# Optimization experiments

Hardware: AMD Instinct MI355X
Metric: run time of the kernel (lower is better)

Reference implementation:

```python
import jax, jax.numpy as jnp
import numpy as np

H_DIM = 64; GRID = 8; G = GRID * GRID; NEIGH = 2.0
ATT = 1024; EMB = 4
S = 32; P = 64; B = S * P


def setup_inputs() -> dict:
    key = jax.random.key(0)
    ks = jax.random.split(key, 20)
    bounds = jnp.arange(0, B + 1, P, dtype=jnp.int32)
    seq_start_end = jnp.stack([bounds[:-1], bounds[1:]], axis=1)  # (S,2) uniform scenes
    def lin(k, fan_in, shape):
        return jax.random.normal(k, shape, jnp.float32) / np.sqrt(fan_in)
    return {
        "h_states": jax.random.normal(ks[0], (1, B, H_DIM), jnp.float32),
        "seq_start_end": seq_start_end,
        "end_pos": jax.random.uniform(ks[1], (B, 2), jnp.float32) * 4.0,
        "rel_pos": jax.random.normal(ks[2], (B, 2), jnp.float32),
        # Attention_Decoder params
        "W_enc": lin(ks[3], H_DIM, (H_DIM, ATT)), "b_enc": jnp.zeros((ATT,), jnp.float32),
        "W_dec": lin(ks[4], H_DIM, (H_DIM, ATT)), "b_dec": jnp.zeros((ATT,), jnp.float32),
        "w_full": lin(ks[5], ATT, (ATT,)), "b_full": jnp.zeros((), jnp.float32),
        "W_embed": lin(ks[6], 4, (4, EMB)), "b_embed": jnp.zeros((EMB,), jnp.float32),
        "W_out": lin(ks[7], H_DIM + EMB, (H_DIM + EMB, ATT)), "b_out": jnp.zeros((ATT,), jnp.float32),
        # mlp_pool params (Linear -> BatchNorm -> ReLU)
        "W_mlp": lin(ks[8], ATT, (ATT, ATT)), "b_mlp": jnp.zeros((ATT,), jnp.float32),
        "bn_gamma": jnp.ones((ATT,), jnp.float32), "bn_beta": jnp.zeros((ATT,), jnp.float32),
    }


def social_pool(h, end_pos):
    # h: (B, H), end_pos: (B, 2); uniform scenes S x P
    pos = end_pos.reshape(S, P, 2)
    hid = h.reshape(S, P, H_DIM)
    ax = pos[:, :, None, 0]; ay = pos[:, :, None, 1]  # anchor (S,P,1)
    ox = pos[:, None, :, 0]; oy = pos[:, None, :, 1]  # other  (S,1,P)
    half = NEIGH / 2
    tl_x = ax - half; tl_y = ay + half
    br_x = ax + half; br_y = ay - half
    cell_x = jnp.floor((ox - tl_x) / NEIGH * GRID)
    cell_y = jnp.floor((tl_y - oy) / NEIGH * GRID)
    grid = (cell_x + cell_y * GRID).astype(jnp.int32)  # (S,P,P)
    oob = (ox >= br_x) | (ox <= tl_x) | (oy >= tl_y) | (oy <= br_y)
    oob = oob | jnp.eye(P, dtype=bool)[None]  # self-pairs excluded (within_bound[0::P+1]=1)
    anchor_off = (jnp.arange(P, dtype=jnp.int32) * G)[None, :, None]
    idx = jnp.where(oob, 0, grid + 1 + anchor_off)  # slot 0 = dump slot
    seq_off = (jnp.arange(S, dtype=jnp.int32) * (P * G + 1))[:, None, None]
    flat_idx = (idx + seq_off).reshape(-1)
    vals = jnp.broadcast_to(hid[:, None, :, :], (S, P, P, H_DIM)).reshape(-1, H_DIM)
    buf = jnp.zeros((S * (P * G + 1), H_DIM), h.dtype).at[flat_idx].add(vals)
    buf = buf.reshape(S, P * G + 1, H_DIM)[:, 1:, :]  # drop dump slot per scene
    return buf.reshape(B, G, H_DIM)


def reference(h_states, seq_start_end, end_pos, rel_pos,
              W_enc, b_enc, W_dec, b_dec, w_full, b_full,
              W_embed, b_embed, W_out, b_out, W_mlp, b_mlp, bn_gamma, bn_beta):
    del seq_start_end  # uniform scene layout baked into S, P
    h = h_states.reshape(-1, H_DIM)                      # (B, H)
    enc = social_pool(h, end_pos)                        # (B, G, H)
    dec_a = h @ W_dec + b_dec                            # (B, ATT)
    enc_a = jnp.einsum('bgh,ha->bga', enc, W_enc) + b_enc
    scores = jax.nn.relu(enc_a + dec_a[:, None, :]) @ w_full + b_full  # (B, G)
    alpha = jax.nn.softmax(scores, axis=-1)
    ctx = jnp.einsum('bg,bgh->bh', alpha, enc)           # (B, H)
    embed_info = jnp.concatenate([end_pos, rel_pos], axis=1)  # (B, 4)
    emb = jax.nn.relu(embed_info @ W_embed + b_embed)
    out = jax.nn.relu(jnp.concatenate([ctx, emb], axis=1) @ W_out + b_out)  # (B, ATT)
    # mlp_pool: Linear -> BatchNorm1d (training-mode batch stats) -> ReLU
    x = out @ W_mlp + b_mlp
    mu = jnp.mean(x, axis=0)
    var = jnp.var(x, axis=0)
    x = (x - mu) * jax.lax.rsqrt(var + 1e-5) * bn_gamma + bn_beta
    return jax.nn.relu(x)
```

## Files before the change

kernel.cpp:

```cpp
#include <hip/hip_runtime.h>
#include <hip/hip_bf16.h>
#include <math.h>

#define H_DIM 64
#define G 64
#define ATT 1024
#define EMB 4
#define P 64
#define BB 2048
#define MAXROWS 129088
#define PREP_BLOCKS (2048 + 16 + 16 + 16 + 256)

typedef __attribute__((ext_vector_type(8))) short short8;
typedef __attribute__((ext_vector_type(4))) float floatx4;

__device__ inline ushort f2bf(float v) {
    __hip_bfloat16 b = __float2bfloat16(v);
    return *(ushort*)&b;
}
__device__ inline float bf2f(ushort u) {
    union { float f; unsigned u32; } x;
    x.u32 = ((unsigned)u) << 16;
    return x.f;
}

__global__ __launch_bounds__(256) void prep_kernel(const float* __restrict__ h,
                                                   const float* __restrict__ end_pos,
                                                   const float* __restrict__ W_enc,
                                                   const float* __restrict__ W_dec,
                                                   const float* __restrict__ W_out,
                                                   const float* __restrict__ W_mlp,
                                                   ushort* __restrict__ enc,
                                                   ushort* __restrict__ h_bf,
                                                   ushort* __restrict__ Wte,
                                                   ushort* __restrict__ Wdt,
                                                   ushort* __restrict__ Wot,
                                                   ushort* __restrict__ Wt,
                                                   int* __restrict__ rowidx,
                                                   int* __restrict__ cntA,
                                                   int* __restrict__ baseA,
                                                   int* __restrict__ counter) {
    __shared__ float cellp[2][G][H_DIM];
    __shared__ float tileT[64][65];
    __shared__ unsigned long long hitsS[2];
    __shared__ int baseS;

    int blk = blockIdx.x;
    int t = threadIdx.x;

    if (blk < 2048) {
        int b = blk, s = b >> 6, i = b & 63;
        int w = t >> 6, lane = t & 63;
        float* cp = &cellp[0][0][0];
        #pragma unroll
        for (int idx = 0; idx < 8; ++idx)
            *(float4*)&cp[(t + 256 * idx) * 4] = (float4){0.f, 0.f, 0.f, 0.f};
        if (w == 3) h_bf[(size_t)b * 64 + lane] = f2bf(h[(size_t)b * 64 + lane]);
        __syncthreads();

        float ax = end_pos[2 * b], ay = end_pos[2 * b + 1];
        float tlx = ax - 1.f, tly = ay + 1.f, brx = ax + 1.f, bry = ay - 1.f;
        const float* hseq = h + (size_t)s * P * H_DIM;
        const float* pseq = end_pos + (size_t)s * P * 2;

        if (w < 2) {
            unsigned long long hits = 0ull;
            for (int jj = 0; jj < 32; ++jj) {
                int j = w * 32 + jj;
                float ox = pseq[2 * j], oy = pseq[2 * j + 1];
                bool oob = (ox >= brx) || (ox <= tlx) || (oy >= tly) || (oy <= bry) || (j == i);
                if (!oob) {
                    int cx = (int)floorf((ox - tlx) / 2.0f * 8.0f);
                    int cy = (int)floorf((tly - oy) / 2.0f * 8.0f);
                    int g = cx + cy * 8;
                    hits |= (1ull << g);
                    cellp[w][g][lane] += hseq[j * H_DIM + lane];
                }
            }
            if (lane == 0) hitsS[w] = hits;
        }
        __syncthreads();
        unsigned long long uh = hitsS[0] | hitsS[1];
        int n_nz = __popcll(uh);
        if (t == 0) {
            int bs = atomicAdd(counter, n_nz);
            baseS = bs; cntA[b] = n_nz; baseA[b] = bs;
        }
        __syncthreads();
        int base = baseS;
        for (int g = w; g < 64; g += 4) {
            if ((uh >> g) & 1ull) {
                int slot = __popcll(uh & ((1ull << g) - 1ull));
                enc[((size_t)(b * G + g)) * H_DIM + lane] =
                    f2bf(cellp[0][g][lane] + cellp[1][g][lane]);
                if (lane == 0) rowidx[base + slot] = b * G + g;
            }
        }
    } else if (blk < 2064) {
        int n0 = (blk - 2048) * 64;
        #pragma unroll
        for (int idx = 0; idx < 16; ++idx) {
            int flat = t + 256 * idx;
            int k = flat >> 6, c = flat & 63;
            tileT[k][c] = W_enc[(size_t)k * ATT + n0 + c];
        }
        __syncthreads();
        #pragma unroll
        for (int idx = 0; idx < 16; ++idx) {
            int flat = t + 256 * idx;
            int n = flat >> 6, k = flat & 63;
            Wte[(size_t)(n0 + n) * 64 + k] = f2bf(tileT[k][n]);
        }
    } else if (blk < 2080) {
        int n0 = (blk - 2064) * 64;
        #pragma unroll
        for (int idx = 0; idx < 16; ++idx) {
            int flat = t + 256 * idx;
            int k = flat >> 6, c = flat & 63;
            tileT[k][c] = W_dec[(size_t)k * ATT + n0 + c];
        }
        __syncthreads();
        #pragma unroll
        for (int idx = 0; idx < 16; ++idx) {
            int flat = t + 256 * idx;
            int n = flat >> 6, k = flat & 63;
            Wdt[(size_t)(n0 + n) * 64 + k] = f2bf(tileT[k][n]);
        }
    } else if (blk < 2096) {
        int n0 = (blk - 2080) * 64;
        int n = t & 63, kg = t >> 6;
        #pragma unroll
        for (int kk = 0; kk < 24; ++kk) {
            int k = kg * 24 + kk;
            float v = (k < 68) ? W_out[(size_t)k * ATT + n0 + n] : 0.f;
            Wot[(size_t)(n0 + n) * 96 + k] = f2bf(v);
        }
    } else {
        int idx2 = blk - 2096;
        int k0 = (idx2 & 15) * 64, n0 = (idx2 >> 4) * 64;
        #pragma unroll
        for (int idx = 0; idx < 16; ++idx) {
            int flat = t + 256 * idx;
            int r = flat >> 6, c = flat & 63;
            tileT[r][c] = W_mlp[(size_t)(k0 + r) * ATT + n0 + c];
        }
        __syncthreads();
        #pragma unroll
        for (int idx = 0; idx < 16; ++idx) {
            int flat = t + 256 * idx;
            int r = flat >> 6, c = flat & 63;
            Wt[(size_t)(n0 + r) * ATT + k0 + c] = f2bf(tileT[c][r]);
        }
    }
}

__global__ __launch_bounds__(256) void dec_mfma_kernel(const ushort* __restrict__ A,
                                                       const ushort* __restrict__ Bt,
                                                       const float* __restrict__ b_dec,
                                                       const float* __restrict__ b_enc,
                                                       const float* __restrict__ w_full,
                                                       float* __restrict__ dec_r,
                                                       float* __restrict__ s_empty) {
    int t = threadIdx.x;
    int w = t >> 6, lane = t & 63;
    int lm = lane & 15, q = lane >> 4;
    int m0 = blockIdx.x * 64, n1 = blockIdx.y * 128;
    __shared__ __align__(16) ushort Asm[64][72];
    __shared__ __align__(16) ushort Bsm[128][72];

    #pragma unroll
    for (int i = 0; i < 4; ++i) {
        int flat = t + 256 * i;
        int r = flat >> 4, c4 = (flat & 15) * 4;
        *(uint2*)&Asm[r][c4] = *(const uint2*)&A[(size_t)(m0 + r) * 64 + c4];
    }
    #pragma unroll
    for (int i = 0; i < 8; ++i) {
        int flat = t + 256 * i;
        int r = flat >> 4, c4 = (flat & 15) * 4;
        *(uint2*)&Bsm[r][c4] = *(const uint2*)&Bt[(size_t)(n1 + r) * 64 + c4];
    }
    __syncthreads();

    floatx4 acc[4][2];
    #pragma unroll
    for (int mt = 0; mt < 4; ++mt)
        #pragma unroll
        for (int nt = 0; nt < 2; ++nt) acc[mt][nt] = (floatx4){0.f, 0.f, 0.f, 0.f};

    #pragma unroll
    for (int ks = 0; ks < 64; ks += 32) {
        short8 af[4], bfr[2];
        #pragma unroll
        for (int mt = 0; mt < 4; ++mt)
            af[mt] = *(const short8*)&Asm[mt * 16 + lm][ks + q * 8];
        #pragma unroll
        for (int nt = 0; nt < 2; ++nt)
            bfr[nt] = *(const short8*)&Bsm[w * 32 + nt * 16 + lm][ks + q * 8];
        #pragma unroll
        for (int mt = 0; mt < 4; ++mt)
            #pragma unroll
            for (int nt = 0; nt < 2; ++nt)
                acc[mt][nt] = __builtin_amdgcn_mfma_f32_16x16x32_bf16(af[mt], bfr[nt], acc[mt][nt], 0, 0, 0);
    }

    float part[4][4];
    #pragma unroll
    for (int mt = 0; mt < 4; ++mt)
        #pragma unroll
        for (int r = 0; r < 4; ++r) part[mt][r] = 0.f;

    #pragma unroll
    for (int nt = 0; nt < 2; ++nt) {
        int col = n1 + w * 32 + nt * 16 + lm;
        float bcol = b_dec[col] + b_enc[col];
        float wf = w_full[col];
        #pragma unroll
        for (int mt = 0; mt < 4; ++mt)
            #pragma unroll
            for (int r = 0; r < 4; ++r) {
                int row = m0 + mt * 16 + q * 4 + r;
                float v = acc[mt][nt][r] + bcol;
                dec_r[(size_t)row * ATT + col] = v;
                part[mt][r] += fmaxf(v, 0.f) * wf;
            }
    }
    #pragma unroll
    for (int mt = 0; mt < 4; ++mt)
        #pragma unroll
        for (int r = 0; r < 4; ++r) {
            float v = part[mt][r];
            v += __shfl_xor(v, 1); v += __shfl_xor(v, 2);
            v += __shfl_xor(v, 4); v += __shfl_xor(v, 8);
            part[mt][r] = v;
        }
    if (lm == 0) {
        #pragma unroll
        for (int mt = 0; mt < 4; ++mt)
            #pragma unroll
            for (int r = 0; r < 4; ++r)
                atomicAdd(&s_empty[m0 + mt * 16 + q * 4 + r], part[mt][r]);
    }
}

__global__ __launch_bounds__(256) void scoresC_mfma_kernel(const ushort* __restrict__ enc,
                                                           const int* __restrict__ rowidx,
                                                           const int* __restrict__ counter,
                                                           const float* __restrict__ dec_r,
                                                           const ushort* __restrict__ Wte,
                                                           const float* __restrict__ w_full,
                                                           const float* __restrict__ b_full,
                                                           float* __restrict__ score_c) {
    int M = counter[0];
    int row0 = blockIdx.x * 64;
    if (row0 >= M) return;
    int t = threadIdx.x;
    int w = t >> 6, lane = t & 63;
    int lm = lane & 15, q = lane >> 4;

    __shared__ __align__(16) ushort AS[64][72];
    __shared__ __align__(16) ushort BS[256][72];
    __shared__ int rowS[64];
    __shared__ float redS[4][64];

    if (t < 64) rowS[t] = (row0 + t < M) ? rowidx[row0 + t] : 0;
    __syncthreads();
    #pragma unroll
    for (int i = 0; i < 4; ++i) {
        int flat = t + 256 * i;
        int r = flat >> 4, c4 = (flat & 15) * 4;
        *(uint2*)&AS[r][c4] = *(const uint2*)&enc[(size_t)rowS[r] * 64 + c4];
    }
    int bbr[16];
    #pragma unroll
    for (int mt = 0; mt < 4; ++mt)
        #pragma unroll
        for (int r = 0; r < 4; ++r)
            bbr[mt * 4 + r] = rowS[mt * 16 + q * 4 + r] >> 6;

    float part[4][4];
    #pragma unroll
    for (int mt = 0; mt < 4; ++mt)
        #pragma unroll
        for (int r = 0; r < 4; ++r) part[mt][r] = 0.f;

    for (int c = 0; c < 4; ++c) {
        __syncthreads();
        #pragma unroll
        for (int i = 0; i < 16; ++i) {
            int flat = t + 256 * i;
            int r = flat >> 4, c4 = (flat & 15) * 4;
            *(uint2*)&BS[r][c4] = *(const uint2*)&Wte[(size_t)(c * 256 + r) * 64 + c4];
        }
        __syncthreads();

        floatx4 acc[4][4];
        #pragma unroll
        for (int mt = 0; mt < 4; ++mt)
            #pragma unroll
            for (int nt = 0; nt < 4; ++nt) acc[mt][nt] = (floatx4){0.f, 0.f, 0.f, 0.f};

        #pragma unroll
        for (int ks = 0; ks < 64; ks += 32) {
            short8 af[4], bfr[4];
            #pragma unroll
            for (int mt = 0; mt < 4; ++mt)
                af[mt] = *(const short8*)&AS[mt * 16 + lm][ks + q * 8];
            #pragma unroll
            for (int nt = 0; nt < 4; ++nt)
                bfr[nt] = *(const short8*)&BS[w * 64 + nt * 16 + lm][ks + q * 8];
            #pragma unroll
            for (int mt = 0; mt < 4; ++mt)
                #pragma unroll
                for (int nt = 0; nt < 4; ++nt)
                    acc[mt][nt] = __builtin_amdgcn_mfma_f32_16x16x32_bf16(af[mt], bfr[nt], acc[mt][nt], 0, 0, 0);
        }

        int colbase = c * 256 + w * 64;
        #pragma unroll
        for (int nt = 0; nt < 4; ++nt) {
            int col = colbase + nt * 16 + lm;
            float wf = w_full[col];
            #pragma unroll
            for (int mt = 0; mt < 4; ++mt)
                #pragma unroll
                for (int r = 0; r < 4; ++r) {
                    float v = acc[mt][nt][r] + dec_r[(size_t)bbr[mt * 4 + r] * ATT + col];
                    part[mt][r] += fmaxf(v, 0.f) * wf;
                }
        }
    }
    #pragma unroll
    for (int mt = 0; mt < 4; ++mt)
        #pragma unroll
        for (int r = 0; r < 4; ++r) {
            float v = part[mt][r];
            v += __shfl_xor(v, 1); v += __shfl_xor(v, 2);
            v += __shfl_xor(v, 4); v += __shfl_xor(v, 8);
            part[mt][r] = v;
        }
    if (lm == 0) {
        #pragma unroll
        for (int mt = 0; mt < 4; ++mt)
            #pragma unroll
            for (int r = 0; r < 4; ++r)
                redS[w][mt * 16 + q * 4 + r] = part[mt][r];
    }
    __syncthreads();
    if (t < 64) {
        int row = row0 + t;
        if (row < M)
            score_c[row] = redS[0][t] + redS[1][t] + redS[2][t] + redS[3][t] + b_full[0];
    }
}

__global__ __launch_bounds__(64) void softmax_ctx_kernel(const float* __restrict__ score_c,
                                                         const int* __restrict__ rowidx,
                                                         const int* __restrict__ cntA,
                                                         const int* __restrict__ baseA,
                                                         const float* __restrict__ s_empty,
                                                         const ushort* __restrict__ enc,
                                                         const float* __restrict__ end_pos,
                                                         const float* __restrict__ rel_pos,
                                                         const float* __restrict__ W_embed,
                                                         const float* __restrict__ b_embed,
                                                         const float* __restrict__ b_full,
                                                         ushort* __restrict__ ctx_bf) {
    int b = blockIdx.x, t = threadIdx.x;
    int cnt = cntA[b], base = baseA[b];
    float se = s_empty[b] + b_full[0];
    float sc = se;
    int ri = 0;
    if (t < cnt) { sc = score_c[base + t]; ri = rowidx[base + t]; }
    float mx = sc;
    #pragma unroll
    for (int o = 32; o > 0; o >>= 1) mx = fmaxf(mx, __shfl_xor(mx, o));
    float e = expf(sc - mx);
    float ssum = e;
    #pragma unroll
    for (int o = 32; o > 0; o >>= 1) ssum += __shfl_xor(ssum, o);
    __shared__ float aS[G];
    __shared__ int rS[G];
    aS[t] = e / ssum;
    rS[t] = ri;
    __syncthreads();
    float ctx = 0.f;
    for (int i = 0; i < cnt; ++i)
        ctx += aS[i] * bf2f(enc[(size_t)rS[i] * H_DIM + t]);
    ctx_bf[(size_t)b * 96 + t] = f2bf(ctx);
    if (t < EMB) {
        float e0 = end_pos[2*b], e1 = end_pos[2*b+1], e2 = rel_pos[2*b], e3 = rel_pos[2*b+1];
        float v = b_embed[t] + e0 * W_embed[0*EMB + t] + e1 * W_embed[1*EMB + t]
                             + e2 * W_embed[2*EMB + t] + e3 * W_embed[3*EMB + t];
        ctx_bf[(size_t)b * 96 + 64 + t] = f2bf(v > 0.f ? v : 0.f);
    }
    if (t < 28) ctx_bf[(size_t)b * 96 + 68 + t] = 0;
}

__global__ __launch_bounds__(256) void out_mfma_kernel(const ushort* __restrict__ A,
                                                       const ushort* __restrict__ Bt,
                                                       const float* __restrict__ bias,
                                                       ushort* __restrict__ out) {
    int t = threadIdx.x;
    int w = t >> 6, lane = t & 63;
    int lm = lane & 15, q = lane >> 4;
    int m0 = blockIdx.x * 64, n1 = blockIdx.y * 128;
    __shared__ __align__(16) ushort Asm[64][104];
    __shared__ __align__(16) ushort Bsm[128][104];

    {
        int r = t >> 2, pp = t & 3;
        #pragma unroll
        for (int ii = 0; ii < 3; ++ii) {
            int c8 = (pp * 3 + ii) * 8;
            *(uint4*)&Asm[r][c8] = *(const uint4*)&A[(size_t)(m0 + r) * 96 + c8];
        }
    }
    {
        int r = t >> 1, pp = t & 1;
        #pragma unroll
        for (int ii = 0; ii < 6; ++ii) {
            int c8 = (pp * 6 + ii) * 8;
            *(uint4*)&Bsm[r][c8] = *(const uint4*)&Bt[(size_t)(n1 + r) * 96 + c8];
        }
    }
    __syncthreads();

    floatx4 acc[4][2];
    #pragma unroll
    for (int mt = 0; mt < 4; ++mt)
        #pragma unroll
        for (int nt = 0; nt < 2; ++nt) acc[mt][nt] = (floatx4){0.f, 0.f, 0.f, 0.f};

    #pragma unroll
    for (int ks = 0; ks < 96; ks += 32) {
        short8 af[4], bfr[2];
        #pragma unroll
        for (int mt = 0; mt < 4; ++mt)
            af[mt] = *(const short8*)&Asm[mt * 16 + lm][ks + q * 8];
        #pragma unroll
        for (int nt = 0; nt < 2; ++nt)
            bfr[nt] = *(const short8*)&Bsm[w * 32 + nt * 16 + lm][ks + q * 8];
        #pragma unroll
        for (int mt = 0; mt < 4; ++mt)
            #pragma unroll
            for (int nt = 0; nt < 2; ++nt)
                acc[mt][nt] = __builtin_amdgcn_mfma_f32_16x16x32_bf16(af[mt], bfr[nt], acc[mt][nt], 0, 0, 0);
    }
    #pragma unroll
    for (int nt = 0; nt < 2; ++nt) {
        int col = n1 + w * 32 + nt * 16 + lm;
        float bv = bias[col];
        #pragma unroll
        for (int mt = 0; mt < 4; ++mt)
            #pragma unroll
            for (int r = 0; r < 4; ++r) {
                int row = m0 + mt * 16 + q * 4 + r;
                out[(size_t)row * ATT + col] = f2bf(fmaxf(acc[mt][nt][r] + bv, 0.f));
            }
    }
}

__global__ __launch_bounds__(256) void mlp_mfma_kernel(const ushort* __restrict__ A,
                                                       const ushort* __restrict__ Bt,
                                                       const float* __restrict__ bias,
                                                       float* __restrict__ X,
                                                       float* __restrict__ sums) {
    int t = threadIdx.x;
    int w = t >> 6, lane = t & 63;
    int lm = lane & 15, q = lane >> 4;
    int m0 = blockIdx.x * 64, n1 = blockIdx.y * 128;
    __shared__ __align__(16) ushort Asm[64][72];
    __shared__ __align__(16) ushort Bsm[128][72];

    floatx4 acc[4][2];
    #pragma unroll
    for (int mt = 0; mt < 4; ++mt)
        #pragma unroll
        for (int nt = 0; nt < 2; ++nt) acc[mt][nt] = (floatx4){0.f, 0.f, 0.f, 0.f};

    for (int k0 = 0; k0 < 1024; k0 += 64) {
        __syncthreads();
        #pragma unroll
        for (int i = 0; i < 4; ++i) {
            int flat = t + 256 * i;
            int r = flat >> 4, c4 = (flat & 15) * 4;
            *(uint2*)&Asm[r][c4] = *(const uint2*)&A[(size_t)(m0 + r) * 1024 + k0 + c4];
        }
        #pragma unroll
        for (int i = 0; i < 8; ++i) {
            int flat = t + 256 * i;
            int r = flat >> 4, c4 = (flat & 15) * 4;
            *(uint2*)&Bsm[r][c4] = *(const uint2*)&Bt[(size_t)(n1 + r) * 1024 + k0 + c4];
        }
        __syncthreads();
        #pragma unroll
        for (int ks = 0; ks < 64; ks += 32) {
            short8 af[4], bfr[2];
            #pragma unroll
            for (int mt = 0; mt < 4; ++mt)
                af[mt] = *(const short8*)&Asm[mt * 16 + lm][ks + q * 8];
            #pragma unroll
            for (int nt = 0; nt < 2; ++nt)
                bfr[nt] = *(const short8*)&Bsm[w * 32 + nt * 16 + lm][ks + q * 8];
            #pragma unroll
            for (int mt = 0; mt < 4; ++mt)
                #pragma unroll
                for (int nt = 0; nt < 2; ++nt)
                    acc[mt][nt] = __builtin_amdgcn_mfma_f32_16x16x32_bf16(af[mt], bfr[nt], acc[mt][nt], 0, 0, 0);
        }
    }
    #pragma unroll
    for (int nt = 0; nt < 2; ++nt) {
        int col = n1 + w * 32 + nt * 16 + lm;
        float bv = bias[col];
        float s1 = 0.f, s2 = 0.f;
        #pragma unroll
        for (int mt = 0; mt < 4; ++mt)
            #pragma unroll
            for (int r = 0; r < 4; ++r) {
                int row = m0 + mt * 16 + q * 4 + r;
                float v = acc[mt][nt][r] + bv;
                X[(size_t)row * 1024 + col] = v;
                s1 += v; s2 += v * v;
            }
        s1 += __shfl_xor(s1, 16); s1 += __shfl_xor(s1, 32);
        s2 += __shfl_xor(s2, 16); s2 += __shfl_xor(s2, 32);
        if (q == 0) {
            atomicAdd(&sums[col], s1);
            atomicAdd(&sums[ATT + col], s2);
        }
    }
}

__global__ __launch_bounds__(256) void bn_kernel(const float* __restrict__ X,
                                                 const float* __restrict__ sums,
                                                 const float* __restrict__ gamma,
                                                 const float* __restrict__ beta,
                                                 float* __restrict__ out) {
    size_t i = (size_t)blockIdx.x * 256 + threadIdx.x;
    int f = (int)(i & 1023);
    float mu = sums[f] * (1.f / BB);
    float var = sums[ATT + f] * (1.f / BB) - mu * mu;
    float v = (X[i] - mu) * rsqrtf(var + 1e-5f) * gamma[f] + beta[f];
    out[i] = v > 0.f ? v : 0.f;
}

extern "C" void kernel_launch(void* const* d_in, const int* in_sizes, int n_in,
                              void* d_out, int out_size, void* d_ws, size_t ws_size,
                              hipStream_t stream) {
    const float* h        = (const float*)d_in[0];
    const float* end_pos  = (const float*)d_in[2];
    const float* rel_pos  = (const float*)d_in[3];
    const float* W_enc    = (const float*)d_in[4];
    const float* b_enc    = (const float*)d_in[5];
    const float* W_dec    = (const float*)d_in[6];
    const float* b_dec    = (const float*)d_in[7];
    const float* w_full   = (const float*)d_in[8];
    const float* b_full   = (const float*)d_in[9];
    const float* W_embed  = (const float*)d_in[10];
    const float* b_embed  = (const float*)d_in[11];
    const float* W_out    = (const float*)d_in[12];
    const float* b_out    = (const float*)d_in[13];
    const float* W_mlp    = (const float*)d_in[14];
    const float* b_mlp    = (const float*)d_in[15];
    const float* bn_gamma = (const float*)d_in[16];
    const float* bn_beta  = (const float*)d_in[17];

    float* ws = (float*)d_ws;
    ushort* enc     = (ushort*)ws;
    ushort* h_bf    = (ushort*)(ws + 4194304);
    ushort* Wte     = (ushort*)(ws + 4259840);
    ushort* Wdt     = (ushort*)(ws + 4292608);
    ushort* Wot     = (ushort*)(ws + 4325376);
    ushort* Wt      = (ushort*)(ws + 4374528);
    ushort* ctx_bf  = (ushort*)(ws + 4898816);
    ushort* out_bf  = (ushort*)(ws + 4997120);
    float*  x       = ws + 6045696;
    float*  dec_r   = ws + 8388608;
    int*    rowidx  = (int*)(ws + 10485760);
    float*  score_c = ws + 10616832;
    int*    cntA    = (int*)(ws + 10747904);
    int*    baseA   = (int*)(ws + 10749952);
    int*    counter = (int*)(ws + 10752000);
    float*  s_empty = ws + 10752064;
    float*  sums    = ws + 10754112;

    hipMemsetAsync(counter, 0, (64 + 2048 + 2048) * sizeof(float), stream);

    prep_kernel<<<PREP_BLOCKS, 256, 0, stream>>>(h, end_pos, W_enc, W_dec, W_out, W_mlp,
                                                 enc, h_bf, Wte, Wdt, Wot, Wt,
                                                 rowidx, cntA, baseA, counter);
    dec_mfma_kernel<<<dim3(32, 8), 256, 0, stream>>>(h_bf, Wdt, b_dec, b_enc, w_full, dec_r, s_empty);
    scoresC_mfma_kernel<<<MAXROWS / 64, 256, 0, stream>>>(enc, rowidx, counter, dec_r, Wte,
                                                          w_full, b_full, score_c);
    softmax_ctx_kernel<<<BB, 64, 0, stream>>>(score_c, rowidx, cntA, baseA, s_empty, enc,
                                              end_pos, rel_pos, W_embed, b_embed, b_full, ctx_bf);
    out_mfma_kernel<<<dim3(32, 8), 256, 0, stream>>>(ctx_bf, Wot, b_out, out_bf);
    mlp_mfma_kernel<<<dim3(32, 8), 256, 0, stream>>>(out_bf, Wt, b_mlp, x, sums);
    bn_kernel<<<8192, 256, 0, stream>>>(x, sums, bn_gamma, bn_beta, (float*)d_out);
}
```

Baseline: 202.1 us.

## Compute social pooling per wavefront with ballot/shuffle instead of shared-memory cells

After: 195.7 us. 3.2% less time.

```diff
diff --git a/kernel.cpp b/kernel.cpp
--- a/kernel.cpp
+++ b/kernel.cpp
@@ -9,7 +9,7 @@
 #define P 64
 #define BB 2048
 #define MAXROWS 129088
-#define PREP_BLOCKS (2048 + 16 + 16 + 16 + 256)
+#define PREP_BLOCKS (512 + 16 + 16 + 16 + 256)
 
 typedef __attribute__((ext_vector_type(8))) short short8;
 typedef __attribute__((ext_vector_type(4))) float floatx4;
@@ -40,64 +40,57 @@
                                                    int* __restrict__ cntA,
                                                    int* __restrict__ baseA,
                                                    int* __restrict__ counter) {
-    __shared__ float cellp[2][G][H_DIM];
     __shared__ float tileT[64][65];
-    __shared__ unsigned long long hitsS[2];
-    __shared__ int baseS;
 
     int blk = blockIdx.x;
     int t = threadIdx.x;
 
-    if (blk < 2048) {
-        int b = blk, s = b >> 6, i = b & 63;
-        int w = t >> 6, lane = t & 63;
-        float* cp = &cellp[0][0][0];
-        #pragma unroll
-        for (int idx = 0; idx < 8; ++idx)
-            *(float4*)&cp[(t + 256 * idx) * 4] = (float4){0.f, 0.f, 0.f, 0.f};
-        if (w == 3) h_bf[(size_t)b * 64 + lane] = f2bf(h[(size_t)b * 64 + lane]);
-        __syncthreads();
-
-        float ax = end_pos[2 * b], ay = end_pos[2 * b + 1];
+    if (blk < 512) {
+        int wv = t >> 6, lane = t & 63;
+        int b = blk * 4 + wv;
+        int s = b >> 6, i = b & 63;
+        const float* pseq = end_pos + (size_t)s * P * 2;
+        const float* hrow = h + (size_t)s * P * H_DIM;
+
+        float2 pj = ((const float2*)pseq)[lane];
+        float ax = __shfl(pj.x, i), ay = __shfl(pj.y, i);
         float tlx = ax - 1.f, tly = ay + 1.f, brx = ax + 1.f, bry = ay - 1.f;
-        const float* hseq = h + (size_t)s * P * H_DIM;
-        const float* pseq = end_pos + (size_t)s * P * 2;
-
-        if (w < 2) {
-            unsigned long long hits = 0ull;
-            for (int jj = 0; jj < 32; ++jj) {
-                int j = w * 32 + jj;
-                float ox = pseq[2 * j], oy = pseq[2 * j + 1];
-                bool oob = (ox >= brx) || (ox <= tlx) || (oy >= tly) || (oy <= bry) || (j == i);
-                if (!oob) {
-                    int cx = (int)floorf((ox - tlx) / 2.0f * 8.0f);
-                    int cy = (int)floorf((tly - oy) / 2.0f * 8.0f);
-                    int g = cx + cy * 8;
-                    hits |= (1ull << g);
-                    cellp[w][g][lane] += hseq[j * H_DIM + lane];
-                }
+        bool oob = (pj.x >= brx) || (pj.x <= tlx) || (pj.y >= tly) || (pj.y <= bry) || (lane == i);
+        int cx = (int)floorf((pj.x - tlx) * 4.0f);
+        int cy = (int)floorf((tly - pj.y) * 4.0f);
+        int g = cx + cy * 8;
+
+        unsigned long long hitmask = __ballot(!oob);
+        unsigned long long m = hitmask, cellmask = 0ull;
+        while (m) {
+            int j = __builtin_ctzll(m); m &= m - 1;
+            int gj = __shfl(g, j);
+            cellmask |= 1ull << gj;
+        }
+        int n_nz = __popcll(cellmask);
+        int base = 0;
+        if (lane == 0) base = atomicAdd(counter, n_nz);
+        base = __shfl(base, 0);
+        if (lane == 0) { cntA[b] = n_nz; baseA[b] = base; }
+
+        h_bf[(size_t)b * 64 + lane] = f2bf(h[(size_t)b * 64 + lane]);
+
+        unsigned long long cm = cellmask;
+        int slot = 0;
+        while (cm) {
+            int gg = __builtin_ctzll(cm); cm &= cm - 1;
+            unsigned long long jm = __ballot((!oob) && (g == gg));
+            float sum = 0.f;
+            while (jm) {
+                int j = __builtin_ctzll(jm); jm &= jm - 1;
+                sum += hrow[j * H_DIM + lane];
             }
-            if (lane == 0) hitsS[w] = hits;
-        }
-        __syncthreads();
-        unsigned long long uh = hitsS[0] | hitsS[1];
-        int n_nz = __popcll(uh);
-        if (t == 0) {
-            int bs = atomicAdd(counter, n_nz);
-            baseS = bs; cntA[b] = n_nz; baseA[b] = bs;
-        }
-        __syncthreads();
-        int base = baseS;
-        for (int g = w; g < 64; g += 4) {
-            if ((uh >> g) & 1ull) {
-                int slot = __popcll(uh & ((1ull << g) - 1ull));
-                enc[((size_t)(b * G + g)) * H_DIM + lane] =
-                    f2bf(cellp[0][g][lane] + cellp[1][g][lane]);
-                if (lane == 0) rowidx[base + slot] = b * G + g;
-            }
-        }
-    } else if (blk < 2064) {
-        int n0 = (blk - 2048) * 64;
+            enc[((size_t)(b * G + gg)) * H_DIM + lane] = f2bf(sum);
+            if (lane == 0) rowidx[base + slot] = b * G + gg;
+            ++slot;
+        }
+    } else if (blk < 528) {
+        int n0 = (blk - 512) * 64;
         #pragma unroll
         for (int idx = 0; idx < 16; ++idx) {
             int flat = t + 256 * idx;
@@ -111,8 +104,8 @@
             int n = flat >> 6, k = flat & 63;
             Wte[(size_t)(n0 + n) * 64 + k] = f2bf(tileT[k][n]);
         }
-    } else if (blk < 2080) {
-        int n0 = (blk - 2064) * 64;
+    } else if (blk < 544) {
+        int n0 = (blk - 528) * 64;
         #pragma unroll
         for (int idx = 0; idx < 16; ++idx) {
             int flat = t + 256 * idx;
@@ -126,8 +119,8 @@
             int n = flat >> 6, k = flat & 63;
             Wdt[(size_t)(n0 + n) * 64 + k] = f2bf(tileT[k][n]);
         }
-    } else if (blk < 2096) {
-        int n0 = (blk - 2080) * 64;
+    } else if (blk < 560) {
+        int n0 = (blk - 544) * 64;
         int n = t & 63, kg = t >> 6;
         #pragma unroll
         for (int kk = 0; kk < 24; ++kk) {
@@ -136,7 +129,7 @@
             Wot[(size_t)(n0 + n) * 96 + k] = f2bf(v);
         }
     } else {
-        int idx2 = blk - 2096;
+        int idx2 = blk - 560;
         int k0 = (idx2 & 15) * 64, n0 = (idx2 >> 4) * 64;
         #pragma unroll
         for (int idx = 0; idx < 16; ++idx) {
```
